# Optimization experiments

Measured on AMD Instinct MI355X. Metric: run time of the kernel, lower is better.

## Reference

```python
import jax, jax.numpy as jnp
import numpy as np
import math

DIM = 1024
NUM_HEADS = 16
HEAD_DIM = DIM // NUM_HEADS
LOGIT_SCALE_MAX = math.log(1.0 / 0.01)
EPS = 1e-12  # F.normalize eps


def setup_inputs() -> dict:
    key = jax.random.key(0)
    ks = jax.random.split(key, 4)
    L, N, C = 1024, 8, DIM
    scale = HEAD_DIM ** -0.5
    x = jax.random.normal(ks[0], (L, N, C), dtype=jnp.float32)
    in_proj_weight = jax.random.normal(ks[1], (3 * C, C), dtype=jnp.float32) * scale
    in_proj_bias = jnp.zeros((3 * C,), dtype=jnp.float32)
    logit_scale = jnp.full((NUM_HEADS, 1, 1), math.log(10.0), dtype=jnp.float32)
    head_scale = jnp.ones((NUM_HEADS, 1, 1), dtype=jnp.float32)
    out_w = jax.random.normal(ks[2], (C, C), dtype=jnp.float32) * (C ** -0.5)
    out_b = jax.random.normal(ks[3], (C,), dtype=jnp.float32) * 0.01
    return {"x": x, "in_proj_weight": in_proj_weight, "in_proj_bias": in_proj_bias,
            "logit_scale": logit_scale, "head_scale": head_scale,
            "out_w": out_w, "out_b": out_b}


def _l2_normalize(t):
    # matches F.normalize(t, dim=-1): t / max(||t||_2, eps)
    n = jnp.sqrt(jnp.sum(t * t, axis=-1, keepdims=True))
    return t / jnp.maximum(n, EPS)


def reference(x, in_proj_weight, in_proj_bias, logit_scale, head_scale, out_w, out_b):
    L, N, C = x.shape
    H, hd = NUM_HEADS, HEAD_DIM
    qkv = x @ in_proj_weight.T + in_proj_bias          # (L, N, 3C)
    q, k, v = jnp.split(qkv, 3, axis=-1)               # each (L, N, C)

    def to_heads(t):  # (L, N, C) -> (N, H, L, hd)
        return t.reshape(L, N, H, hd).transpose(1, 2, 0, 3)

    q, k, v = to_heads(q), to_heads(k), to_heads(v)
    # scaled-cosine attention
    ls = jnp.exp(jnp.minimum(logit_scale, LOGIT_SCALE_MAX))  # (H,1,1) broadcasts
    attn = jnp.einsum('nhld,nhmd->nhlm', _l2_normalize(q), _l2_normalize(k)) * ls
    attn = jax.nn.softmax(attn, axis=-1)               # (N, H, L, L)
    o = jnp.einsum('nhlm,nhmd->nhld', attn, v)         # (N, H, L, hd)
    o = o * head_scale                                  # per-head scale
    o = o.transpose(2, 0, 1, 3).reshape(L, N, C)       # back to (L, N, C)
    return o @ out_w.T + out_b
```

## Files before the change

kernel.cpp:

```cpp
#include <hip/hip_runtime.h>
#include <hip/hip_bf16.h>

typedef __hip_bfloat16 bf16;
typedef __attribute__((ext_vector_type(8))) short bf16x8;
typedef __attribute__((ext_vector_type(4))) float f32x4;

#define LOGIT_MAX 4.6051702f

__device__ __forceinline__ float4 load4(const float* p) { return *(const float4*)p; }

__device__ __forceinline__ void store4bf(bf16* p, float4 v) {
    union { bf16 b[4]; uint2 u; } t;
    t.b[0] = __float2bfloat16(v.x); t.b[1] = __float2bfloat16(v.y);
    t.b[2] = __float2bfloat16(v.z); t.b[3] = __float2bfloat16(v.w);
    *(uint2*)p = t.u;
}

__device__ __forceinline__ void async16(const bf16* g, const bf16* lds) {
    __builtin_amdgcn_global_load_lds(
        (const __attribute__((address_space(1))) void*)g,
        (__attribute__((address_space(3))) void*)lds, 16, 0, 0);
}

__global__ __launch_bounds__(256) void prep_kernel(
    const void* __restrict__ x, const void* __restrict__ w_in, const void* __restrict__ out_w,
    const void* __restrict__ b_in, const void* __restrict__ out_b,
    const void* __restrict__ ls, const void* __restrict__ hs,
    bf16* __restrict__ xb, bf16* __restrict__ wb, bf16* __restrict__ owb,
    float* __restrict__ smallf, int* __restrict__ flag)
{
    __shared__ int cnt_lds[4];
    const unsigned short* xs = (const unsigned short*)x;
    int c = 0;
    for (int i = threadIdx.x; i < 4096; i += 256) {
        const unsigned e = (xs[i] >> 7) & 0xFF;
        if (e >= 0x90) c++;
    }
#pragma unroll
    for (int off = 32; off > 0; off >>= 1) c += __shfl_down(c, off, 64);
    if ((threadIdx.x & 63) == 0) cnt_lds[threadIdx.x >> 6] = c;
    __syncthreads();
    const int f = (cnt_lds[0] + cnt_lds[1] + cnt_lds[2] + cnt_lds[3] > 64) ? 1 : 0;

    if (blockIdx.x == 0) {
        if (threadIdx.x == 0) *flag = f;
        for (int idx = threadIdx.x; idx < 4128; idx += 256) {
            float v;
            if (f) {
                if (idx < 3072)      v = ((const float*)b_in)[idx];
                else if (idx < 4096) v = ((const float*)out_b)[idx - 3072];
                else if (idx < 4112) v = expf(fminf(((const float*)ls)[idx - 4096], LOGIT_MAX));
                else                 v = ((const float*)hs)[idx - 4112];
            } else {
                if (idx < 3072)      v = __bfloat162float(((const bf16*)b_in)[idx]);
                else if (idx < 4096) v = __bfloat162float(((const bf16*)out_b)[idx - 3072]);
                else if (idx < 4112) v = expf(fminf(__bfloat162float(((const bf16*)ls)[idx - 4096]), LOGIT_MAX));
                else                 v = __bfloat162float(((const bf16*)hs)[idx - 4112]);
            }
            smallf[idx] = v;
        }
    }
    if (f != 1) return;
    const size_t NX = 8388608, NW = 3145728, NO = 1048576;
    const size_t t0   = ((size_t)blockIdx.x * 256 + threadIdx.x) * 4;
    const size_t step = (size_t)gridDim.x * 256 * 4;
    for (size_t i = t0; i < NX; i += step) store4bf(xb + i, load4((const float*)x + i));
    for (size_t i = t0; i < NW; i += step) store4bf(wb + i, load4((const float*)w_in + i));
    for (size_t i = t0; i < NO; i += step) store4bf(owb + i, load4((const float*)out_w + i));
}

__global__ __launch_bounds__(256, 4) void qkv_gemm_mfma_kernel(
    const int* __restrict__ flag,
    const bf16* __restrict__ Xws, const bf16* __restrict__ Wws,
    const bf16* __restrict__ Xdir, const bf16* __restrict__ Wdir,
    const float* __restrict__ bias_f,
    bf16* __restrict__ q, bf16* __restrict__ k, bf16* __restrict__ vt)
{
    const bf16* X = (*flag) ? Xws : Xdir;
    const bf16* W = (*flag) ? Wws : Wdir;
    __shared__ bf16 A_lds[128 * 64];
    __shared__ bf16 B_lds[128 * 64];
    const int tid  = threadIdx.x;
    const int w    = tid >> 6;
    const int lane = tid & 63;
    const int l16  = lane & 15, quad = lane >> 4;
    const int wm   = w >> 1, wn = w & 1;
    const int row0 = blockIdx.y * 128;
    const int col0 = blockIdx.x * 128;
    const int sr   = lane >> 3, sc = lane & 7;
    const int scg  = sc ^ sr;

    f32x4 acc[4][4] = {};

    for (int kt = 0; kt < 1024; kt += 64) {
        __syncthreads();
#pragma unroll
        for (int i = 0; i < 4; i++) {
            const int br = w * 32 + i * 8;
            async16(X + (size_t)(row0 + br + sr) * 1024 + kt + scg * 8, &A_lds[br * 64]);
            async16(W + (size_t)(col0 + br + sr) * 1024 + kt + scg * 8, &B_lds[br * 64]);
        }
        __syncthreads();

#pragma unroll
        for (int kh = 0; kh < 2; kh++) {
            bf16x8 af[4], bf[4];
#pragma unroll
            for (int mt = 0; mt < 4; mt++) {
                const int row = wm * 64 + mt * 16 + l16;
                af[mt] = *(const bf16x8*)&A_lds[row * 64 + (((quad + kh * 4) ^ (row & 7)) * 8)];
            }
#pragma unroll
            for (int nt = 0; nt < 4; nt++) {
                const int row = wn * 64 + nt * 16 + l16;
                bf[nt] = *(const bf16x8*)&B_lds[row * 64 + (((quad + kh * 4) ^ (row & 7)) * 8)];
            }
#pragma unroll
            for (int mt = 0; mt < 4; mt++)
#pragma unroll
                for (int nt = 0; nt < 4; nt++)
                    acc[mt][nt] = __builtin_amdgcn_mfma_f32_16x16x32_bf16(af[mt], bf[nt], acc[mt][nt], 0, 0, 0);
        }
    }

    const int cbase = col0 + wn * 64;
    const int part  = cbase >> 10;
    const int h     = (cbase & 1023) >> 6;
    float bias[4];
#pragma unroll
    for (int nt = 0; nt < 4; nt++) bias[nt] = bias_f[cbase + nt * 16 + l16];

    if (part < 2) {
        bf16* dst0 = (part == 0) ? q : k;
#pragma unroll
        for (int mt = 0; mt < 4; mt++) {
#pragma unroll
            for (int rg = 0; rg < 4; rg++) {
                const int r = row0 + wm * 64 + mt * 16 + quad * 4 + rg;
                const int l = r >> 3, nn = r & 7;
                float val[4]; float ss = 0.f;
#pragma unroll
                for (int nt = 0; nt < 4; nt++) {
                    val[nt] = acc[mt][nt][rg] + bias[nt];
                    ss += val[nt] * val[nt];
                }
                ss += __shfl_xor(ss, 1); ss += __shfl_xor(ss, 2);
                ss += __shfl_xor(ss, 4); ss += __shfl_xor(ss, 8);
                const float inv = 1.f / fmaxf(sqrtf(ss), 1e-12f);
                bf16* dp = dst0 + ((size_t)((nn * 16 + h) * 1024 + l)) * 64;
#pragma unroll
                for (int nt = 0; nt < 4; nt++)
                    dp[nt * 16 + l16] = __float2bfloat16(val[nt] * inv);
            }
        }
    } else {
#pragma unroll
        for (int mt = 0; mt < 4; mt++) {
#pragma unroll
            for (int rg = 0; rg < 4; rg++) {
                const int r = row0 + wm * 64 + mt * 16 + quad * 4 + rg;
                const int l = r >> 3, nn = r & 7;
#pragma unroll
                for (int nt = 0; nt < 4; nt++) {
                    const int d = nt * 16 + l16;
                    vt[((size_t)((nn * 16 + h) * 64 + d)) * 1024 + l] =
                        __float2bfloat16(acc[mt][nt][rg] + bias[nt]);
                }
            }
        }
    }
}

__global__ __launch_bounds__(256, 4) void attn_mfma_kernel(
    const bf16* __restrict__ q, const bf16* __restrict__ k,
    const bf16* __restrict__ vt, const float* __restrict__ scale_f,
    bf16* __restrict__ o)
{
    __shared__ bf16 K_lds[64][64];
    __shared__ bf16 Vt_lds[64][64];
    __shared__ bf16 P_lds[4][32][72];
    __shared__ float l_lds[4][32];

    const int bid  = blockIdx.x;
    const int qt   = bid >> 7;
    const int nh   = bid & 127;
    const int h    = nh & 15;
    const int n    = nh >> 4;
    const int tid  = threadIdx.x;
    const int w    = tid >> 6;
    const int lane = tid & 63;
    const int l16  = lane & 15;
    const int quad = lane >> 4;

    const size_t base = (size_t)nh * (1024 * 64);
    const float ls   = scale_f[4096 + h];
    const float hs   = scale_f[4112 + h];
    const float lsl2 = ls * 1.4426950408889634f;

    bf16x8 qf[2][2];
#pragma unroll
    for (int u = 0; u < 2; u++) {
        const int qrow = qt * 128 + w * 32 + u * 16 + l16;
        const bf16* qp = q + base + (size_t)qrow * 64 + quad * 8;
        qf[u][0] = *(const bf16x8*)qp;
        qf[u][1] = *(const bf16x8*)(qp + 32);
    }

    f32x4 o_acc[2][4] = {};
    float l_part[2] = {0.f, 0.f};

    const int sr = lane >> 3;
    const int sc = lane & 7;

    for (int j0 = 0; j0 < 1024; j0 += 64) {
        __syncthreads();
#pragma unroll
        for (int half = 0; half < 2; half++) {
            const int br  = w * 16 + half * 8;
            const int row = br + sr;
            const int cg  = sc ^ (row & 7);
            async16(k  + base + (size_t)(j0 + row) * 64 + cg * 8, &K_lds[br][0]);
            async16(vt + base + (size_t)row * 1024 + j0 + cg * 8, &Vt_lds[br][0]);
        }
        __syncthreads();

        f32x4 s8[2][4];
#pragma unroll
        for (int s = 0; s < 4; s++) {
            const int krow = s * 16 + l16;
            const int swz  = krow & 7;
            const bf16x8 kf0 = *(const bf16x8*)&K_lds[krow][(quad ^ swz) * 8];
            const bf16x8 kf1 = *(const bf16x8*)&K_lds[krow][((quad + 4) ^ swz) * 8];
#pragma unroll
            for (int u = 0; u < 2; u++) {
                f32x4 a = {};
                a = __builtin_amdgcn_mfma_f32_16x16x32_bf16(kf0, qf[u][0], a, 0, 0, 0);
                a = __builtin_amdgcn_mfma_f32_16x16x32_bf16(kf1, qf[u][1], a, 0, 0, 0);
                s8[u][s] = a;
            }
        }

#pragma unroll
        for (int u = 0; u < 2; u++) {
#pragma unroll
            for (int s = 0; s < 4; s++) {
                union { bf16 b[4]; uint2 uu; } pk;
                float sum = 0.f;
#pragma unroll
                for (int r = 0; r < 4; r++) {
                    const float p = exp2f(fmaf(s8[u][s][r], lsl2, -lsl2));
                    pk.b[r] = __float2bfloat16(p);
                    sum += p;
                }
                l_part[u] += sum;
                *(uint2*)&P_lds[w][u * 16 + l16][s * 16 + quad * 4] = pk.uu;
            }
        }

        bf16x8 pf[2][2];
#pragma unroll
        for (int u = 0; u < 2; u++) {
            pf[u][0] = *(const bf16x8*)&P_lds[w][u * 16 + l16][quad * 8];
            pf[u][1] = *(const bf16x8*)&P_lds[w][u * 16 + l16][32 + quad * 8];
        }
#pragma unroll
        for (int ds = 0; ds < 4; ds++) {
            const int vrow = ds * 16 + l16;
            const int swz  = vrow & 7;
            const bf16x8 vf0 = *(const bf16x8*)&Vt_lds[vrow][(quad ^ swz) * 8];
            const bf16x8 vf1 = *(const bf16x8*)&Vt_lds[vrow][((quad + 4) ^ swz) * 8];
#pragma unroll
            for (int u = 0; u < 2; u++) {
                o_acc[u][ds] = __builtin_amdgcn_mfma_f32_16x16x32_bf16(pf[u][0], vf0, o_acc[u][ds], 0, 0, 0);
                o_acc[u][ds] = __builtin_amdgcn_mfma_f32_16x16x32_bf16(pf[u][1], vf1, o_acc[u][ds], 0, 0, 0);
            }
        }
    }

#pragma unroll
    for (int u = 0; u < 2; u++) {
        float v = l_part[u];
        v += __shfl_xor(v, 16);
        v += __shfl_xor(v, 32);
        l_lds[w][u * 16 + l16] = v;
    }

#pragma unroll
    for (int u = 0; u < 2; u++) {
#pragma unroll
        for (int r = 0; r < 4; r++) {
            const float inv = hs / l_lds[w][u * 16 + quad * 4 + r];
            const int row_l = qt * 128 + w * 32 + u * 16 + quad * 4 + r;
            bf16* dst = o + ((size_t)row_l * 8 + n) * 1024 + h * 64 + l16;
#pragma unroll
            for (int ds = 0; ds < 4; ds++)
                dst[ds * 16] = __float2bfloat16(o_acc[u][ds][r] * inv);
        }
    }
}

__global__ __launch_bounds__(256, 4) void out_gemm_mfma_kernel(
    const int* __restrict__ flag,
    const bf16* __restrict__ A,
    const bf16* __restrict__ Bws, const bf16* __restrict__ Bdir,
    const float* __restrict__ bias_f,
    float* __restrict__ outf, bf16* __restrict__ outb)
{
    const int f = *flag;
    const bf16* B = f ? Bws : Bdir;
    __shared__ bf16 A_lds[128 * 64];
    __shared__ bf16 B_lds[128 * 64];
    const int tid  = threadIdx.x;
    const int w    = tid >> 6;
    const int lane = tid & 63;
    const int l16  = lane & 15, quad = lane >> 4;
    const int wm   = w >> 1, wn = w & 1;
    const int row0 = blockIdx.y * 128;
    const int col0 = blockIdx.x * 128;
    const int sr   = lane >> 3, sc = lane & 7;
    const int scg  = sc ^ sr;

    f32x4 acc[4][4] = {};

    for (int kt = 0; kt < 1024; kt += 64) {
        __syncthreads();
#pragma unroll
        for (int i = 0; i < 4; i++) {
            const int br = w * 32 + i * 8;
            async16(A + (size_t)(row0 + br + sr) * 1024 + kt + scg * 8, &A_lds[br * 64]);
            async16(B + (size_t)(col0 + br + sr) * 1024 + kt + scg * 8, &B_lds[br * 64]);
        }
        __syncthreads();

#pragma unroll
        for (int kh = 0; kh < 2; kh++) {
            bf16x8 af[4], bf[4];
#pragma unroll
            for (int mt = 0; mt < 4; mt++) {
                const int row = wm * 64 + mt * 16 + l16;
                af[mt] = *(const bf16x8*)&A_lds[row * 64 + (((quad + kh * 4) ^ (row & 7)) * 8)];
            }
#pragma unroll
            for (int nt = 0; nt < 4; nt++) {
                const int row = wn * 64 + nt * 16 + l16;
                bf[nt] = *(const bf16x8*)&B_lds[row * 64 + (((quad + kh * 4) ^ (row & 7)) * 8)];
            }
#pragma unroll
            for (int mt = 0; mt < 4; mt++)
#pragma unroll
                for (int nt = 0; nt < 4; nt++)
                    acc[mt][nt] = __builtin_amdgcn_mfma_f32_16x16x32_bf16(af[mt], bf[nt], acc[mt][nt], 0, 0, 0);
        }
    }

#pragma unroll
    for (int mt = 0; mt < 4; mt++) {
        const int rbase = row0 + wm * 64 + mt * 16 + quad * 4;
#pragma unroll
        for (int nt = 0; nt < 4; nt++) {
            const int c = col0 + wn * 64 + nt * 16 + l16;
            const float bias = bias_f[c];
#pragma unroll
            for (int rg = 0; rg < 4; rg++) {
                const float v = acc[mt][nt][rg] + bias;
                const size_t idx = (size_t)(rbase + rg) * 1024 + c;
                if (f) outf[idx] = v; else outb[idx] = __float2bfloat16(v);
            }
        }
    }
}

extern "C" void kernel_launch(void* const* d_in, const int* in_sizes, int n_in,
                              void* d_out, int out_size, void* d_ws, size_t ws_size,
                              hipStream_t stream)
{
    const size_t SEG = (size_t)8 * 16 * 1024 * 64;
    bf16* qn  = (bf16*)d_ws;
    bf16* kn  = qn + SEG;
    bf16* vt  = kn + SEG;
    bf16* ow  = vt + SEG;
    bf16* xb  = ow + SEG;
    bf16* wb  = xb + SEG;
    bf16* owb = wb + 3145728;
    float* smallf = (float*)(owb + 1048576);
    int*   flag   = (int*)(smallf + 4128);

    prep_kernel<<<2048, 256, 0, stream>>>(
        d_in[0], d_in[1], d_in[5], d_in[2], d_in[6], d_in[3], d_in[4],
        xb, wb, owb, smallf, flag);

    qkv_gemm_mfma_kernel<<<dim3(3072 / 128, 8192 / 128), 256, 0, stream>>>(
        flag, xb, wb, (const bf16*)d_in[0], (const bf16*)d_in[1], smallf, qn, kn, vt);

    attn_mfma_kernel<<<dim3(128 * 8), 256, 0, stream>>>(qn, kn, vt, smallf, ow);

    out_gemm_mfma_kernel<<<dim3(1024 / 128, 8192 / 128), 256, 0, stream>>>(
        flag, ow, owb, (const bf16*)d_in[5], smallf + 3072,
        (float*)d_out, (bf16*)d_out);
}
```

Before: 280.8 us.

## Fuse fp32-to-bf16 conversion of X into QKV GEMM tile loads

Stops materialising a bf16 copy of the 8M-element input X in the prep kernel. The QKV GEMM now loads fp32 X directly, converts it to bf16 in registers and stores it swizzled into LDS, which removes a full write and re-read of X. The cost is losing the async global-to-LDS path for the A tile, and each X tile is converted repeatedly across the 24 column blocks. Launch bounds drop to 3 waves per SIMD and the prep grid shrinks to match the smaller copy workload.

```diff
diff --git a/kernel.cpp b/kernel.cpp
--- a/kernel.cpp
+++ b/kernel.cpp
@@ -16,6 +16,15 @@
     *(uint2*)p = t.u;
 }
 
+__device__ __forceinline__ uint4 pack8bf(float4 a, float4 b) {
+    union { bf16 h[8]; uint4 u; } t;
+    t.h[0] = __float2bfloat16(a.x); t.h[1] = __float2bfloat16(a.y);
+    t.h[2] = __float2bfloat16(a.z); t.h[3] = __float2bfloat16(a.w);
+    t.h[4] = __float2bfloat16(b.x); t.h[5] = __float2bfloat16(b.y);
+    t.h[6] = __float2bfloat16(b.z); t.h[7] = __float2bfloat16(b.w);
+    return t.u;
+}
+
 __device__ __forceinline__ void async16(const bf16* g, const bf16* lds) {
     __builtin_amdgcn_global_load_lds(
         (const __attribute__((address_space(1))) void*)g,
@@ -26,7 +35,7 @@
     const void* __restrict__ x, const void* __restrict__ w_in, const void* __restrict__ out_w,
     const void* __restrict__ b_in, const void* __restrict__ out_b,
     const void* __restrict__ ls, const void* __restrict__ hs,
-    bf16* __restrict__ xb, bf16* __restrict__ wb, bf16* __restrict__ owb,
+    bf16* __restrict__ wb, bf16* __restrict__ owb,
     float* __restrict__ smallf, int* __restrict__ flag)
 {
     __shared__ int cnt_lds[4];
@@ -61,23 +70,22 @@
         }
     }
     if (f != 1) return;
-    const size_t NX = 8388608, NW = 3145728, NO = 1048576;
+    const size_t NW = 3145728, NO = 1048576;
     const size_t t0   = ((size_t)blockIdx.x * 256 + threadIdx.x) * 4;
     const size_t step = (size_t)gridDim.x * 256 * 4;
-    for (size_t i = t0; i < NX; i += step) store4bf(xb + i, load4((const float*)x + i));
     for (size_t i = t0; i < NW; i += step) store4bf(wb + i, load4((const float*)w_in + i));
     for (size_t i = t0; i < NO; i += step) store4bf(owb + i, load4((const float*)out_w + i));
 }
 
-__global__ __launch_bounds__(256, 4) void qkv_gemm_mfma_kernel(
+__global__ __launch_bounds__(256, 3) void qkv_gemm_mfma_kernel(
     const int* __restrict__ flag,
-    const bf16* __restrict__ Xws, const bf16* __restrict__ Wws,
-    const bf16* __restrict__ Xdir, const bf16* __restrict__ Wdir,
+    const float* __restrict__ Xf, const bf16* __restrict__ Xdir,
+    const bf16* __restrict__ Wws, const bf16* __restrict__ Wdir,
     const float* __restrict__ bias_f,
     bf16* __restrict__ q, bf16* __restrict__ k, bf16* __restrict__ vt)
 {
-    const bf16* X = (*flag) ? Xws : Xdir;
-    const bf16* W = (*flag) ? Wws : Wdir;
+    const int f = *flag;
+    const bf16* W = f ? Wws : Wdir;
     __shared__ bf16 A_lds[128 * 64];
     __shared__ bf16 B_lds[128 * 64];
     const int tid  = threadIdx.x;
@@ -94,10 +102,24 @@
 
     for (int kt = 0; kt < 1024; kt += 64) {
         __syncthreads();
+        if (f) {
+#pragma unroll
+            for (int i = 0; i < 4; i++) {
+                const int row = w * 32 + i * 8 + sr;
+                const float* gp = Xf + (size_t)(row0 + row) * 1024 + kt + scg * 8;
+                const float4 a0 = load4(gp), a1 = load4(gp + 4);
+                *(uint4*)&A_lds[row * 64 + sc * 8] = pack8bf(a0, a1);
+            }
+        } else {
+#pragma unroll
+            for (int i = 0; i < 4; i++) {
+                const int br = w * 32 + i * 8;
+                async16(Xdir + (size_t)(row0 + br + sr) * 1024 + kt + scg * 8, &A_lds[br * 64]);
+            }
+        }
 #pragma unroll
         for (int i = 0; i < 4; i++) {
             const int br = w * 32 + i * 8;
-            async16(X + (size_t)(row0 + br + sr) * 1024 + kt + scg * 8, &A_lds[br * 64]);
             async16(W + (size_t)(col0 + br + sr) * 1024 + kt + scg * 8, &B_lds[br * 64]);
         }
         __syncthreads();
@@ -379,18 +401,18 @@
     bf16* kn  = qn + SEG;
     bf16* vt  = kn + SEG;
     bf16* ow  = vt + SEG;
-    bf16* xb  = ow + SEG;
-    bf16* wb  = xb + SEG;
+    bf16* wb  = ow + SEG;
     bf16* owb = wb + 3145728;
     float* smallf = (float*)(owb + 1048576);
     int*   flag   = (int*)(smallf + 4128);
 
-    prep_kernel<<<2048, 256, 0, stream>>>(
+    prep_kernel<<<512, 256, 0, stream>>>(
         d_in[0], d_in[1], d_in[5], d_in[2], d_in[6], d_in[3], d_in[4],
-        xb, wb, owb, smallf, flag);
+        wb, owb, smallf, flag);
 
     qkv_gemm_mfma_kernel<<<dim3(3072 / 128, 8192 / 128), 256, 0, stream>>>(
-        flag, xb, wb, (const bf16*)d_in[0], (const bf16*)d_in[1], smallf, qn, kn, vt);
+        flag, (const float*)d_in[0], (const bf16*)d_in[0],
+        wb, (const bf16*)d_in[1], smallf, qn, kn, vt);
 
     attn_mfma_kernel<<<dim3(128 * 8), 256, 0, stream>>>(qn, kn, vt, smallf, ow);
 
```

After: 317.5 us. 13.1% more time.
